# Optimization experiments

Hardware: AMD Instinct MI355X
Metric: run time of the kernel (lower is better)

Reference implementation:

```python
import jax, jax.numpy as jnp
import numpy as np

N_NODES = 100000


def gcn_conv(x, src, dst, norm, W, b, n_nodes):
    # x: [N, Din]; src/dst: [E'] (with self-loops); norm: [E']
    h = x @ W  # [N, Dout] dense transform first (PyG GCNConv order)
    msgs = h[src] * norm[:, None]  # gather + degree scaling, [E', Dout]
    out = jax.ops.segment_sum(msgs, dst, num_segments=n_nodes)  # scatter-add
    return out + b


def setup_inputs() -> dict:
    key = jax.random.key(0)
    k_x, k_e, k_w1, k_w2 = jax.random.split(key, 4)
    input_dim, hidden_dim = 256, 128
    n_edges = 1600000
    x = jax.random.normal(k_x, (N_NODES, input_dim), dtype=jnp.float32)
    edge_index = jax.random.randint(k_e, (2, n_edges), 0, N_NODES, dtype=jnp.int64)
    # Glorot-style init for conv weights, zeros bias (PyG defaults)
    s1 = (6.0 / (input_dim + hidden_dim)) ** 0.5
    s2 = (6.0 / (hidden_dim + hidden_dim)) ** 0.5
    W1 = jax.random.uniform(k_w1, (input_dim, hidden_dim), jnp.float32, -s1, s1)
    W2 = jax.random.uniform(k_w2, (hidden_dim, hidden_dim), jnp.float32, -s2, s2)
    b1 = jnp.zeros((hidden_dim,), jnp.float32)
    b2 = jnp.zeros((hidden_dim,), jnp.float32)
    return {"x": x, "edge_index": edge_index, "W1": W1, "b1": b1, "W2": W2, "b2": b2}


def reference(x, edge_index, W1, b1, W2, b2):
    n = x.shape[0]
    loops = jnp.arange(n, dtype=edge_index.dtype)
    src = jnp.concatenate([edge_index[0], loops])  # add self-loops
    dst = jnp.concatenate([edge_index[1], loops])
    # symmetric normalization deg^-1/2 (in-degree including self-loops)
    deg = jax.ops.segment_sum(jnp.ones_like(dst, dtype=x.dtype), dst, num_segments=n)
    dinv = jax.lax.rsqrt(deg)
    norm = dinv[src] * dinv[dst]
    # layer 1: GCNConv -> ReLU (dropout is identity in eval mode)
    h = jax.nn.relu(gcn_conv(x, src, dst, norm, W1, b1, n))
    # layer 2
    h = jax.nn.relu(gcn_conv(h, src, dst, norm, W2, b2, n))
    return h
```

## Files before the change

### kernel.cpp

```cpp
#include <hip/hip_runtime.h>
#include <hip/hip_bf16.h>


#define DIN 256
#define DH 128
#define BKT_SHIFT 9
#define BKT_SZ 512
#define NBKT_MAX 256
#define CAP 10240

typedef __attribute__((ext_vector_type(8))) short short8;
typedef __attribute__((ext_vector_type(4))) float f32x4;
typedef __attribute__((ext_vector_type(2))) unsigned int uint2e;

__device__ __forceinline__ unsigned short f2bf(float f) {
    union { float f; unsigned int i; } c;
    c.f = f;
    unsigned int r = c.i + 0x7FFFu + ((c.i >> 16) & 1u);
    return (unsigned short)(r >> 16);
}
__device__ __forceinline__ float bf_lo(unsigned int u) {
    union { unsigned int i; float f; } c;
    c.i = u << 16;
    return c.f;
}
__device__ __forceinline__ float bf_hi(unsigned int u) {
    union { unsigned int i; float f; } c;
    c.i = u & 0xFFFF0000u;
    return c.f;
}

__global__ __launch_bounds__(256) void cvt_zero_k(const float* __restrict__ W1,
                                                  const float* __restrict__ W2,
                                                  unsigned short* __restrict__ Wt1,
                                                  unsigned short* __restrict__ Wt2,
                                                  int* __restrict__ bcnt, int WTB) {
    int bx = blockIdx.x;
    int t = threadIdx.x;
    if (bx >= WTB) {
        bcnt[t] = 0;
        return;
    }
    int i = bx * 256 + t;
    if (i < 256 * 128) {
        int k = i >> 7, nn = i & 127;
        Wt1[(size_t)nn * 256 + k] = f2bf(W1[i]);
    } else {
        int j = i - 256 * 128;
        int k = j >> 7, nn = j & 127;
        Wt2[(size_t)nn * 128 + k] = f2bf(W2[j]);
    }
}

template <bool A_BF16, bool SCALE>
__device__ __forceinline__ void gemm_body(unsigned short* Bt, int gb,
                                          const void* __restrict__ Av,
                                          const unsigned short* __restrict__ Wt,
                                          const float* __restrict__ dinv,
                                          unsigned short* __restrict__ Hb,
                                          int M, int K) {
    const int t = threadIdx.x;
    const int w = t >> 6;
    const int lane = t & 63;
    const int l15 = lane & 15;
    const int quad = lane >> 4;
    const int row0 = gb * 128 + w * 32;

    const float* Af = (const float*)Av;
    const unsigned short* Ab = (const unsigned short*)Av;

    f32x4 acc[2][8];
#pragma unroll
    for (int rt = 0; rt < 2; ++rt)
#pragma unroll
        for (int ct = 0; ct < 8; ++ct)
#pragma unroll
            for (int j = 0; j < 4; ++j) acc[rt][ct][j] = 0.0f;

    for (int kc = 0; kc < K; kc += 128) {
        if (kc) __syncthreads();
#pragma unroll
        for (int i = 0; i < 8; ++i) {
            int fg = w * 8 + i;
            int ks = fg >> 3, ct = fg & 7;
            int nn = ct * 16 + l15;
            int gk = ks * 32 + quad * 8;
            *(short8*)&Bt[fg * 512 + lane * 8] =
                *(const short8*)(Wt + (size_t)nn * K + kc + gk);
        }
        __syncthreads();
#pragma unroll
        for (int ks = 0; ks < 4; ++ks) {
            int kk = ks * 32 + quad * 8;
            short8 af[2];
#pragma unroll
            for (int rt = 0; rt < 2; ++rt) {
                int row = row0 + rt * 16 + l15;
                if (row < M) {
                    if (A_BF16) {
                        af[rt] = *(const short8*)(Ab + (size_t)row * K + kc + kk);
                    } else {
                        const float* p = Af + (size_t)row * K + kc + kk;
                        float4 x0 = *(const float4*)p;
                        float4 x1 = *(const float4*)(p + 4);
                        af[rt][0] = (short)f2bf(x0.x);
                        af[rt][1] = (short)f2bf(x0.y);
                        af[rt][2] = (short)f2bf(x0.z);
                        af[rt][3] = (short)f2bf(x0.w);
                        af[rt][4] = (short)f2bf(x1.x);
                        af[rt][5] = (short)f2bf(x1.y);
                        af[rt][6] = (short)f2bf(x1.z);
                        af[rt][7] = (short)f2bf(x1.w);
                    }
                } else {
#pragma unroll
                    for (int j = 0; j < 8; ++j) af[rt][j] = 0;
                }
            }
#pragma unroll
            for (int ct = 0; ct < 8; ++ct) {
                short8 bfr = *(const short8*)&Bt[(ks * 8 + ct) * 512 + lane * 8];
                acc[0][ct] = __builtin_amdgcn_mfma_f32_16x16x32_bf16(af[0], bfr, acc[0][ct], 0, 0, 0);
                acc[1][ct] = __builtin_amdgcn_mfma_f32_16x16x32_bf16(af[1], bfr, acc[1][ct], 0, 0, 0);
            }
        }
    }
#pragma unroll
    for (int rt = 0; rt < 2; ++rt)
#pragma unroll
        for (int r = 0; r < 4; ++r) {
            int row = row0 + rt * 16 + quad * 4 + r;
            if (row < M) {
                float dv = SCALE ? dinv[row] : 1.0f;
                unsigned short* o = Hb + (size_t)row * 128 + l15;
#pragma unroll
                for (int ct = 0; ct < 8; ++ct)
                    o[ct * 16] = f2bf(SCALE ? dv * acc[rt][ct][r] : acc[rt][ct][r]);
            }
        }
}

struct SmemFused {
    union {
        unsigned short Bt[16384];
        struct {
            int hist[NBKT_MAX];
            int rstart[NBKT_MAX];
        } bk;
    };
};

__global__ __launch_bounds__(256) void fused1_k(const int* __restrict__ src,
                                                const int* __restrict__ dst,
                                                int* __restrict__ bcnt,
                                                int* __restrict__ tmp, int e, int n,
                                                int NBB,
                                                const float* __restrict__ x,
                                                const unsigned short* __restrict__ Wt1,
                                                unsigned short* __restrict__ hb, int M) {
    __shared__ SmemFused sm;
    int bx = blockIdx.x;
    int t = threadIdx.x;
    if (bx < NBB) {
        int* hist = sm.bk.hist;
        int* rstart = sm.bk.rstart;
        int chunk = (e + NBB - 1) / NBB;
        int beg = bx * chunk, end = min(e, beg + chunk);

        hist[t] = 0;
        __syncthreads();
        for (int i = beg + t; i < end; i += 256) atomicAdd(&hist[dst[i] >> BKT_SHIFT], 1);
        __syncthreads();
        int nbkt = (n + BKT_SZ - 1) >> BKT_SHIFT;
        int h = hist[t];
        if (t < nbkt && h > 0) rstart[t] = atomicAdd(&bcnt[t], h);
        __syncthreads();
        hist[t] = 0;
        __syncthreads();
        for (int i = beg + t; i < end; i += 256) {
            int d = dst[i];
            int b = d >> BKT_SHIFT;
            int o = atomicAdd(&hist[b], 1);
            tmp[(size_t)b * CAP + rstart[b] + o] = src[i] | ((d & (BKT_SZ - 1)) << 20);
        }
        return;
    }
    gemm_body<false, false>(sm.Bt, bx - NBB, x, Wt1, nullptr, hb, M, DIN);
}

__global__ __launch_bounds__(1024) void scatter2_k(const int* __restrict__ tmp,
                                                   const int* __restrict__ bcnt,
                                                   float* __restrict__ dinv,
                                                   int* __restrict__ rowptr,
                                                   int* __restrict__ einfo, int n,
                                                   int nbkt) {
    __shared__ int hist[BKT_SZ];
    __shared__ int scn[BKT_SZ];
    __shared__ int cur[BKT_SZ];
    int b = blockIdx.x;
    int t = threadIdx.x;
    int lo = b << BKT_SHIFT;
    int nn = min(n - lo, BKT_SZ);
    int cnt = bcnt[b];
    const int* rec = tmp + (size_t)b * CAP;

    if (t < 256) scn[t] = (t < nbkt) ? bcnt[t] : 0;
    __syncthreads();
    for (int off = 1; off < 256; off <<= 1) {
        int v = 0;
        if (t < 256 && t >= off) v = scn[t - off];
        __syncthreads();
        if (t < 256) scn[t] += v;
        __syncthreads();
    }
    int bas = scn[b] - cnt;
    if (b == nbkt - 1 && t == 0) rowptr[n] = scn[nbkt - 1];
    __syncthreads();

    if (t < BKT_SZ) hist[t] = 0;
    __syncthreads();
    for (int i = t; i < cnt; i += 1024) atomicAdd(&hist[(rec[i] >> 20) & (BKT_SZ - 1)], 1);
    __syncthreads();
    if (t < BKT_SZ) scn[t] = hist[t];
    __syncthreads();
    for (int off = 1; off < BKT_SZ; off <<= 1) {
        int v = 0;
        if (t < BKT_SZ && t >= off) v = scn[t - off];
        __syncthreads();
        if (t < BKT_SZ) scn[t] += v;
        __syncthreads();
    }
    if (t < nn) {
        int excl = bas + scn[t] - hist[t];
        dinv[lo + t] = 1.0f / sqrtf((float)(hist[t] + 1));
        rowptr[lo + t] = excl;
        cur[t] = excl;
    }
    __syncthreads();
    for (int i = t; i < cnt; i += 1024) {
        int r = rec[i];
        int dlow = (r >> 20) & (BKT_SZ - 1);
        int pos = atomicAdd(&cur[dlow], 1);
        einfo[pos] = r & 0xFFFFF;
    }
}

template <bool SCALE_SRC, bool OUT_BF16>
__global__ __launch_bounds__(256) void agg_k(const unsigned short* __restrict__ Hb,
                                             const int* __restrict__ rowptr,
                                             const int* __restrict__ einfo,
                                             const float* __restrict__ dinv,
                                             const float* __restrict__ bias,
                                             void* __restrict__ out, int n) {
    int v = blockIdx.x * 4 + (threadIdx.x >> 6);
    int lane = threadIdx.x & 63;
    if (v >= n) return;
    int l = lane & 31, half = lane >> 5;
    const uint2* __restrict__ H = (const uint2*)Hb;
    float dv = dinv[v];
    float a0 = 0.f, a1 = 0.f, a2 = 0.f, a3 = 0.f;
    if (half == 0) {
        uint2 hv = H[(size_t)v * 32 + l];
        if (SCALE_SRC) {
            a0 = dv * bf_lo(hv.x); a1 = dv * bf_hi(hv.x);
            a2 = dv * bf_lo(hv.y); a3 = dv * bf_hi(hv.y);
        } else {
            a0 = bf_lo(hv.x); a1 = bf_hi(hv.x);
            a2 = bf_lo(hv.y); a3 = bf_hi(hv.y);
        }
    }
    int end = rowptr[v + 1];
    int i = rowptr[v] + half;
    for (; i + 6 < end; i += 8) {
        int s0 = __builtin_nontemporal_load(&einfo[i]);
        int s1 = __builtin_nontemporal_load(&einfo[i + 2]);
        int s2 = __builtin_nontemporal_load(&einfo[i + 4]);
        int s3 = __builtin_nontemporal_load(&einfo[i + 6]);
        float d0 = 1.f, d1 = 1.f, d2 = 1.f, d3 = 1.f;
        if (SCALE_SRC) { d0 = dinv[s0]; d1 = dinv[s1]; d2 = dinv[s2]; d3 = dinv[s3]; }
        uint2 v0 = H[(size_t)s0 * 32 + l];
        uint2 v1 = H[(size_t)s1 * 32 + l];
        uint2 v2 = H[(size_t)s2 * 32 + l];
        uint2 v3 = H[(size_t)s3 * 32 + l];
        if (SCALE_SRC) {
            a0 = fmaf(d0, bf_lo(v0.x), a0); a1 = fmaf(d0, bf_hi(v0.x), a1);
            a2 = fmaf(d0, bf_lo(v0.y), a2); a3 = fmaf(d0, bf_hi(v0.y), a3);
            a0 = fmaf(d1, bf_lo(v1.x), a0); a1 = fmaf(d1, bf_hi(v1.x), a1);
            a2 = fmaf(d1, bf_lo(v1.y), a2); a3 = fmaf(d1, bf_hi(v1.y), a3);
            a0 = fmaf(d2, bf_lo(v2.x), a0); a1 = fmaf(d2, bf_hi(v2.x), a1);
            a2 = fmaf(d2, bf_lo(v2.y), a2); a3 = fmaf(d2, bf_hi(v2.y), a3);
            a0 = fmaf(d3, bf_lo(v3.x), a0); a1 = fmaf(d3, bf_hi(v3.x), a1);
            a2 = fmaf(d3, bf_lo(v3.y), a2); a3 = fmaf(d3, bf_hi(v3.y), a3);
        } else {
            a0 += bf_lo(v0.x); a1 += bf_hi(v0.x); a2 += bf_lo(v0.y); a3 += bf_hi(v0.y);
            a0 += bf_lo(v1.x); a1 += bf_hi(v1.x); a2 += bf_lo(v1.y); a3 += bf_hi(v1.y);
            a0 += bf_lo(v2.x); a1 += bf_hi(v2.x); a2 += bf_lo(v2.y); a3 += bf_hi(v2.y);
            a0 += bf_lo(v3.x); a1 += bf_hi(v3.x); a2 += bf_lo(v3.y); a3 += bf_hi(v3.y);
        }
    }
    for (; i < end; i += 2) {
        int s = __builtin_nontemporal_load(&einfo[i]);
        float ds = SCALE_SRC ? dinv[s] : 1.f;
        uint2 vv = H[(size_t)s * 32 + l];
        if (SCALE_SRC) {
            a0 = fmaf(ds, bf_lo(vv.x), a0); a1 = fmaf(ds, bf_hi(vv.x), a1);
            a2 = fmaf(ds, bf_lo(vv.y), a2); a3 = fmaf(ds, bf_hi(vv.y), a3);
        } else {
            a0 += bf_lo(vv.x); a1 += bf_hi(vv.x); a2 += bf_lo(vv.y); a3 += bf_hi(vv.y);
        }
    }
    a0 += __shfl_xor(a0, 32);
    a1 += __shfl_xor(a1, 32);
    a2 += __shfl_xor(a2, 32);
    a3 += __shfl_xor(a3, 32);
    if (half == 0) {
        float4 bb = ((const float4*)bias)[l];
        float o0 = fmaxf(fmaf(dv, a0, bb.x), 0.f);
        float o1 = fmaxf(fmaf(dv, a1, bb.y), 0.f);
        float o2 = fmaxf(fmaf(dv, a2, bb.z), 0.f);
        float o3 = fmaxf(fmaf(dv, a3, bb.w), 0.f);
        if (OUT_BF16) {
            uint2e p;
            p.x = (unsigned int)f2bf(o0) | ((unsigned int)f2bf(o1) << 16);
            p.y = (unsigned int)f2bf(o2) | ((unsigned int)f2bf(o3) << 16);
            __builtin_nontemporal_store(p, (uint2e*)out + (size_t)v * 32 + l);
        } else {
            f32x4 o = {o0, o1, o2, o3};
            __builtin_nontemporal_store(o, (f32x4*)out + (size_t)v * 32 + l);
        }
    }
}

__global__ __launch_bounds__(256) void gemm2_k(const unsigned short* __restrict__ A,
                                               const unsigned short* __restrict__ Wt,
                                               const float* __restrict__ dinv,
                                               unsigned short* __restrict__ Hb,
                                               int M, int K) {
    __shared__ unsigned short Bt[16384];
    gemm_body<true, true>(Bt, blockIdx.x, A, Wt, dinv, Hb, M, K);
}

static inline size_t align_up(size_t x, size_t a) { return (x + a - 1) & ~(a - 1); }

extern "C" void kernel_launch(void* const* d_in, const int* in_sizes, int n_in,
                              void* d_out, int out_size, void* d_ws, size_t ws_size,
                              hipStream_t stream) {
    const float* x  = (const float*)d_in[0];
    const int*   ei = (const int*)d_in[1];
    const float* W1 = (const float*)d_in[2];
    const float* b1 = (const float*)d_in[3];
    const float* W2 = (const float*)d_in[4];
    const float* b2 = (const float*)d_in[5];

    const int N = in_sizes[0] / DIN;
    const int E = in_sizes[1] / 2;
    const int* src = ei;
    const int* dst = ei + E;
    const int NBKT = (N + BKT_SZ - 1) >> BKT_SHIFT;

    char* base_p = (char*)d_ws;
    size_t off = 0;
    int* bcnt = (int*)(base_p + off);       off = align_up(off + 256 * 4, 256);
    int* rowptr = (int*)(base_p + off);     off = align_up(off + (size_t)(N + 1) * 4, 256);
    float* dinv = (float*)(base_p + off);   off = align_up(off + (size_t)N * 4, 256);
    int* tmp = (int*)(base_p + off);        off = align_up(off + (size_t)NBKT * CAP * 4, 256);
    int* einfo = (int*)(base_p + off);      off = align_up(off + (size_t)E * 4, 256);
    unsigned short* Wt1 = (unsigned short*)(base_p + off); off = align_up(off + (size_t)128 * 256 * 2, 256);
    unsigned short* Wt2 = (unsigned short*)(base_p + off); off = align_up(off + (size_t)128 * 128 * 2, 256);
    unsigned short* hb  = (unsigned short*)(base_p + off); off = align_up(off + (size_t)N * 128 * 2, 256);
    unsigned short* a1b = (unsigned short*)(base_p + off); off = align_up(off + (size_t)N * 128 * 2, 256);

    float* out = (float*)d_out;

    const int NBB = 512;
    const int WTB = (256 * 128 + 128 * 128 + 255) / 256;
    const int GB = (N + 127) / 128;

    cvt_zero_k<<<WTB + 1, 256, 0, stream>>>(W1, W2, Wt1, Wt2, bcnt, WTB);
    fused1_k<<<NBB + GB, 256, 0, stream>>>(src, dst, bcnt, tmp, E, N, NBB, x, Wt1, hb, N);
    scatter2_k<<<NBKT, 1024, 0, stream>>>(tmp, bcnt, dinv, rowptr, einfo, N, NBKT);
    agg_k<true, true><<<(N + 3) / 4, 256, 0, stream>>>(hb, rowptr, einfo, dinv, b1, a1b, N);
    gemm2_k<<<GB, 256, 0, stream>>>(a1b, Wt2, dinv, hb, N, DH);
    agg_k<false, false><<<(N + 3) / 4, 256, 0, stream>>>(hb, rowptr, einfo, dinv, b2, out, N);
}
```

Baseline: 410.8 us.

## Fuse layer-1 aggregation with layer-2 weight GEMM via per-block MFMA

Merges the first aggregation kernel and the second dense transform: each 4-node block aggregates rows into LDS as bf16 and then runs a 16x16x32 MFMA against W2 (rows padded to 16 with zeros), writing dinv-scaled bf16 H2. This removes the separate GEMM launch and the round trip of the layer-1 activations through global memory. In exchange, only 4 of 16 MFMA rows are useful and every block rereads W2 from global/L2. The bucket-counter zeroing also moves to a hipMemsetAsync, which adds a separate operation on the stream.

```diff
diff --git a/kernel.cpp b/kernel.cpp
--- a/kernel.cpp
+++ b/kernel.cpp
@@ -245,29 +245,127 @@
     }
 }
 
-template <bool SCALE_SRC, bool OUT_BF16>
-__global__ __launch_bounds__(256) void agg_k(const unsigned short* __restrict__ Hb,
-                                             const int* __restrict__ rowptr,
-                                             const int* __restrict__ einfo,
-                                             const float* __restrict__ dinv,
-                                             const float* __restrict__ bias,
-                                             void* __restrict__ out, int n) {
+__global__ __launch_bounds__(256, 8) void agg1_w2_k(const unsigned short* __restrict__ Hb,
+                                                    const int* __restrict__ rowptr,
+                                                    const int* __restrict__ einfo,
+                                                    const float* __restrict__ dinv,
+                                                    const float* __restrict__ bias,
+                                                    const unsigned short* __restrict__ Wt2,
+                                                    unsigned short* __restrict__ G2,
+                                                    int n) {
+    __shared__ unsigned short a1s[16][128];
+    int t = threadIdx.x;
+    int wv = t >> 6;
+    int lane = t & 63;
+    int v0 = blockIdx.x * 4;
+    int v = v0 + wv;
+    {
+        unsigned int* z = (unsigned int*)a1s;
+        for (int i = 256 + t; i < 1024; i += 256) z[i] = 0;
+    }
+    int l = lane & 31, half = lane >> 5;
+    const uint2* __restrict__ H = (const uint2*)Hb;
+    bool valid = (v < n);
+    float o0 = 0.f, o1 = 0.f, o2 = 0.f, o3 = 0.f;
+    if (valid) {
+        float dv = dinv[v];
+        float a0 = 0.f, a1 = 0.f, a2 = 0.f, a3 = 0.f;
+        if (half == 0) {
+            uint2 hv = H[(size_t)v * 32 + l];
+            a0 = dv * bf_lo(hv.x); a1 = dv * bf_hi(hv.x);
+            a2 = dv * bf_lo(hv.y); a3 = dv * bf_hi(hv.y);
+        }
+        int end = rowptr[v + 1];
+        int i = rowptr[v] + half;
+        for (; i + 6 < end; i += 8) {
+            int s0 = __builtin_nontemporal_load(&einfo[i]);
+            int s1 = __builtin_nontemporal_load(&einfo[i + 2]);
+            int s2 = __builtin_nontemporal_load(&einfo[i + 4]);
+            int s3 = __builtin_nontemporal_load(&einfo[i + 6]);
+            float d0 = dinv[s0], d1 = dinv[s1], d2 = dinv[s2], d3 = dinv[s3];
+            uint2 v0g = H[(size_t)s0 * 32 + l];
+            uint2 v1g = H[(size_t)s1 * 32 + l];
+            uint2 v2g = H[(size_t)s2 * 32 + l];
+            uint2 v3g = H[(size_t)s3 * 32 + l];
+            a0 = fmaf(d0, bf_lo(v0g.x), a0); a1 = fmaf(d0, bf_hi(v0g.x), a1);
+            a2 = fmaf(d0, bf_lo(v0g.y), a2); a3 = fmaf(d0, bf_hi(v0g.y), a3);
+            a0 = fmaf(d1, bf_lo(v1g.x), a0); a1 = fmaf(d1, bf_hi(v1g.x), a1);
+            a2 = fmaf(d1, bf_lo(v1g.y), a2); a3 = fmaf(d1, bf_hi(v1g.y), a3);
+            a0 = fmaf(d2, bf_lo(v2g.x), a0); a1 = fmaf(d2, bf_hi(v2g.x), a1);
+            a2 = fmaf(d2, bf_lo(v2g.y), a2); a3 = fmaf(d2, bf_hi(v2g.y), a3);
+            a0 = fmaf(d3, bf_lo(v3g.x), a0); a1 = fmaf(d3, bf_hi(v3g.x), a1);
+            a2 = fmaf(d3, bf_lo(v3g.y), a2); a3 = fmaf(d3, bf_hi(v3g.y), a3);
+        }
+        for (; i < end; i += 2) {
+            int s = __builtin_nontemporal_load(&einfo[i]);
+            float ds = dinv[s];
+            uint2 vv = H[(size_t)s * 32 + l];
+            a0 = fmaf(ds, bf_lo(vv.x), a0); a1 = fmaf(ds, bf_hi(vv.x), a1);
+            a2 = fmaf(ds, bf_lo(vv.y), a2); a3 = fmaf(ds, bf_hi(vv.y), a3);
+        }
+        a0 += __shfl_xor(a0, 32);
+        a1 += __shfl_xor(a1, 32);
+        a2 += __shfl_xor(a2, 32);
+        a3 += __shfl_xor(a3, 32);
+        if (half == 0) {
+            float4 bb = ((const float4*)bias)[l];
+            o0 = fmaxf(fmaf(dv, a0, bb.x), 0.f);
+            o1 = fmaxf(fmaf(dv, a1, bb.y), 0.f);
+            o2 = fmaxf(fmaf(dv, a2, bb.z), 0.f);
+            o3 = fmaxf(fmaf(dv, a3, bb.w), 0.f);
+        }
+    }
+    if (half == 0) {
+        unsigned int p0 = (unsigned int)f2bf(o0) | ((unsigned int)f2bf(o1) << 16);
+        unsigned int p1 = (unsigned int)f2bf(o2) | ((unsigned int)f2bf(o3) << 16);
+        unsigned int* rowp = (unsigned int*)a1s[wv];
+        rowp[l * 2] = p0;
+        rowp[l * 2 + 1] = p1;
+    }
+    __syncthreads();
+    const int l15 = lane & 15;
+    const int quad = lane >> 4;
+    const int ct0 = wv, ct1 = wv + 4;
+    f32x4 acc0 = {0.f, 0.f, 0.f, 0.f};
+    f32x4 acc1 = {0.f, 0.f, 0.f, 0.f};
+#pragma unroll
+    for (int ks = 0; ks < 4; ++ks) {
+        int kk = ks * 32 + quad * 8;
+        short8 afr = *(const short8*)&a1s[l15][kk];
+        short8 b0 = *(const short8*)(Wt2 + (size_t)(ct0 * 16 + l15) * 128 + kk);
+        short8 b1 = *(const short8*)(Wt2 + (size_t)(ct1 * 16 + l15) * 128 + kk);
+        acc0 = __builtin_amdgcn_mfma_f32_16x16x32_bf16(afr, b0, acc0, 0, 0, 0);
+        acc1 = __builtin_amdgcn_mfma_f32_16x16x32_bf16(afr, b1, acc1, 0, 0, 0);
+    }
+    if (quad == 0) {
+#pragma unroll
+        for (int j = 0; j < 4; ++j) {
+            int vj = v0 + j;
+            if (vj < n) {
+                float dj = dinv[vj];
+                G2[(size_t)vj * 128 + ct0 * 16 + l15] = f2bf(dj * acc0[j]);
+                G2[(size_t)vj * 128 + ct1 * 16 + l15] = f2bf(dj * acc1[j]);
+            }
+        }
+    }
+}
+
+__global__ __launch_bounds__(256) void agg2_k(const unsigned short* __restrict__ Hb,
+                                              const int* __restrict__ rowptr,
+                                              const int* __restrict__ einfo,
+                                              const float* __restrict__ dinv,
+                                              const float* __restrict__ bias,
+                                              float* __restrict__ out, int n) {
     int v = blockIdx.x * 4 + (threadIdx.x >> 6);
     int lane = threadIdx.x & 63;
     if (v >= n) return;
     int l = lane & 31, half = lane >> 5;
     const uint2* __restrict__ H = (const uint2*)Hb;
-    float dv = dinv[v];
     float a0 = 0.f, a1 = 0.f, a2 = 0.f, a3 = 0.f;
     if (half == 0) {
         uint2 hv = H[(size_t)v * 32 + l];
-        if (SCALE_SRC) {
-            a0 = dv * bf_lo(hv.x); a1 = dv * bf_hi(hv.x);
-            a2 = dv * bf_lo(hv.y); a3 = dv * bf_hi(hv.y);
-        } else {
-            a0 = bf_lo(hv.x); a1 = bf_hi(hv.x);
-            a2 = bf_lo(hv.y); a3 = bf_hi(hv.y);
-        }
+        a0 = bf_lo(hv.x); a1 = bf_hi(hv.x);
+        a2 = bf_lo(hv.y); a3 = bf_hi(hv.y);
     }
     int end = rowptr[v + 1];
     int i = rowptr[v] + half;
@@ -276,68 +374,34 @@
         int s1 = __builtin_nontemporal_load(&einfo[i + 2]);
         int s2 = __builtin_nontemporal_load(&einfo[i + 4]);
         int s3 = __builtin_nontemporal_load(&einfo[i + 6]);
-        float d0 = 1.f, d1 = 1.f, d2 = 1.f, d3 = 1.f;
-        if (SCALE_SRC) { d0 = dinv[s0]; d1 = dinv[s1]; d2 = dinv[s2]; d3 = dinv[s3]; }
         uint2 v0 = H[(size_t)s0 * 32 + l];
         uint2 v1 = H[(size_t)s1 * 32 + l];
         uint2 v2 = H[(size_t)s2 * 32 + l];
         uint2 v3 = H[(size_t)s3 * 32 + l];
-        if (SCALE_SRC) {
-            a0 = fmaf(d0, bf_lo(v0.x), a0); a1 = fmaf(d0, bf_hi(v0.x), a1);
-            a2 = fmaf(d0, bf_lo(v0.y), a2); a3 = fmaf(d0, bf_hi(v0.y), a3);
-            a0 = fmaf(d1, bf_lo(v1.x), a0); a1 = fmaf(d1, bf_hi(v1.x), a1);
-            a2 = fmaf(d1, bf_lo(v1.y), a2); a3 = fmaf(d1, bf_hi(v1.y), a3);
-            a0 = fmaf(d2, bf_lo(v2.x), a0); a1 = fmaf(d2, bf_hi(v2.x), a1);
-            a2 = fmaf(d2, bf_lo(v2.y), a2); a3 = fmaf(d2, bf_hi(v2.y), a3);
-            a0 = fmaf(d3, bf_lo(v3.x), a0); a1 = fmaf(d3, bf_hi(v3.x), a1);
-            a2 = fmaf(d3, bf_lo(v3.y), a2); a3 = fmaf(d3, bf_hi(v3.y), a3);
-        } else {
-            a0 += bf_lo(v0.x); a1 += bf_hi(v0.x); a2 += bf_lo(v0.y); a3 += bf_hi(v0.y);
-            a0 += bf_lo(v1.x); a1 += bf_hi(v1.x); a2 += bf_lo(v1.y); a3 += bf_hi(v1.y);
-            a0 += bf_lo(v2.x); a1 += bf_hi(v2.x); a2 += bf_lo(v2.y); a3 += bf_hi(v2.y);
-            a0 += bf_lo(v3.x); a1 += bf_hi(v3.x); a2 += bf_lo(v3.y); a3 += bf_hi(v3.y);
-        }
+        a0 += bf_lo(v0.x); a1 += bf_hi(v0.x); a2 += bf_lo(v0.y); a3 += bf_hi(v0.y);
+        a0 += bf_lo(v1.x); a1 += bf_hi(v1.x); a2 += bf_lo(v1.y); a3 += bf_hi(v1.y);
+        a0 += bf_lo(v2.x); a1 += bf_hi(v2.x); a2 += bf_lo(v2.y); a3 += bf_hi(v2.y);
+        a0 += bf_lo(v3.x); a1 += bf_hi(v3.x); a2 += bf_lo(v3.y); a3 += bf_hi(v3.y);
     }
     for (; i < end; i += 2) {
         int s = __builtin_nontemporal_load(&einfo[i]);
-        float ds = SCALE_SRC ? dinv[s] : 1.f;
         uint2 vv = H[(size_t)s * 32 + l];
-        if (SCALE_SRC) {
-            a0 = fmaf(ds, bf_lo(vv.x), a0); a1 = fmaf(ds, bf_hi(vv.x), a1);
-            a2 = fmaf(ds, bf_lo(vv.y), a2); a3 = fmaf(ds, bf_hi(vv.y), a3);
-        } else {
-            a0 += bf_lo(vv.x); a1 += bf_hi(vv.x); a2 += bf_lo(vv.y); a3 += bf_hi(vv.y);
-        }
+        a0 += bf_lo(vv.x); a1 += bf_hi(vv.x); a2 += bf_lo(vv.y); a3 += bf_hi(vv.y);
     }
     a0 += __shfl_xor(a0, 32);
     a1 += __shfl_xor(a1, 32);
     a2 += __shfl_xor(a2, 32);
     a3 += __shfl_xor(a3, 32);
     if (half == 0) {
+        float dv = dinv[v];
         float4 bb = ((const float4*)bias)[l];
         float o0 = fmaxf(fmaf(dv, a0, bb.x), 0.f);
         float o1 = fmaxf(fmaf(dv, a1, bb.y), 0.f);
         float o2 = fmaxf(fmaf(dv, a2, bb.z), 0.f);
         float o3 = fmaxf(fmaf(dv, a3, bb.w), 0.f);
-        if (OUT_BF16) {
-            uint2e p;
-            p.x = (unsigned int)f2bf(o0) | ((unsigned int)f2bf(o1) << 16);
-            p.y = (unsigned int)f2bf(o2) | ((unsigned int)f2bf(o3) << 16);
-            __builtin_nontemporal_store(p, (uint2e*)out + (size_t)v * 32 + l);
-        } else {
-            f32x4 o = {o0, o1, o2, o3};
-            __builtin_nontemporal_store(o, (f32x4*)out + (size_t)v * 32 + l);
-        }
-    }
-}
-
-__global__ __launch_bounds__(256) void gemm2_k(const unsigned short* __restrict__ A,
-                                               const unsigned short* __restrict__ Wt,
-                                               const float* __restrict__ dinv,
-                                               unsigned short* __restrict__ Hb,
-                                               int M, int K) {
-    __shared__ unsigned short Bt[16384];
-    gemm_body<true, true>(Bt, blockIdx.x, A, Wt, dinv, Hb, M, K);
+        f32x4 o = {o0, o1, o2, o3};
+        __builtin_nontemporal_store(o, (f32x4*)out + (size_t)v * 32 + l);
+    }
 }
 
 static inline size_t align_up(size_t x, size_t a) { return (x + a - 1) & ~(a - 1); }
@@ -368,7 +432,7 @@
     unsigned short* Wt1 = (unsigned short*)(base_p + off); off = align_up(off + (size_t)128 * 256 * 2, 256);
     unsigned short* Wt2 = (unsigned short*)(base_p + off); off = align_up(off + (size_t)128 * 128 * 2, 256);
     unsigned short* hb  = (unsigned short*)(base_p + off); off = align_up(off + (size_t)N * 128 * 2, 256);
-    unsigned short* a1b = (unsigned short*)(base_p + off); off = align_up(off + (size_t)N * 128 * 2, 256);
+    unsigned short* g2b = (unsigned short*)(base_p + off); off = align_up(off + (size_t)N * 128 * 2, 256);
 
     float* out = (float*)d_out;
 
@@ -376,10 +440,10 @@
     const int WTB = (256 * 128 + 128 * 128 + 255) / 256;
     const int GB = (N + 127) / 128;
 
-    cvt_zero_k<<<WTB + 1, 256, 0, stream>>>(W1, W2, Wt1, Wt2, bcnt, WTB);
+    hipMemsetAsync(bcnt, 0, 256 * sizeof(int), stream);
+    cvt_zero_k<<<WTB, 256, 0, stream>>>(W1, W2, Wt1, Wt2, bcnt, WTB);
     fused1_k<<<NBB + GB, 256, 0, stream>>>(src, dst, bcnt, tmp, E, N, NBB, x, Wt1, hb, N);
     scatter2_k<<<NBKT, 1024, 0, stream>>>(tmp, bcnt, dinv, rowptr, einfo, N, NBKT);
-    agg_k<true, true><<<(N + 3) / 4, 256, 0, stream>>>(hb, rowptr, einfo, dinv, b1, a1b, N);
-    gemm2_k<<<GB, 256, 0, stream>>>(a1b, Wt2, dinv, hb, N, DH);
-    agg_k<false, false><<<(N + 3) / 4, 256, 0, stream>>>(hb, rowptr, einfo, dinv, b2, out, N);
-}
+    agg1_w2_k<<<(N + 3) / 4, 256, 0, stream>>>(hb, rowptr, einfo, dinv, b1, Wt2, g2b, N);
+    agg2_k<<<(N + 3) / 4, 256, 0, stream>>>(g2b, rowptr, einfo, dinv, b2, out, N);
+}
```

New measurement: 468.0 us. 13.9% more time.

## Replace bucketed two-pass CSR build with global degree count, scan, atomic scatter

Applied to the files above, without the earlier changes.

The CSR construction no longer stages edges in per-bucket temporary buffers. It now counts per-node in-degree with global atomics (fused alongside the first GEMM), runs a per-bucket scan to build rowptr, cursors and dinv, then scatters each source index into place with one global atomic per edge. This drops the intermediate tmp buffer and its second read, but adds many contended global atomics and an extra memset and kernel launch. Edge order within a row also becomes nondeterministic.

```diff
diff --git a/kernel.cpp b/kernel.cpp
--- a/kernel.cpp
+++ b/kernel.cpp
@@ -7,7 +7,6 @@
 #define BKT_SHIFT 9
 #define BKT_SZ 512
 #define NBKT_MAX 256
-#define CAP 10240
 
 typedef __attribute__((ext_vector_type(8))) short short8;
 typedef __attribute__((ext_vector_type(4))) float f32x4;
@@ -30,22 +29,15 @@
     return c.f;
 }
 
-__global__ __launch_bounds__(256) void cvt_zero_k(const float* __restrict__ W1,
-                                                  const float* __restrict__ W2,
-                                                  unsigned short* __restrict__ Wt1,
-                                                  unsigned short* __restrict__ Wt2,
-                                                  int* __restrict__ bcnt, int WTB) {
-    int bx = blockIdx.x;
-    int t = threadIdx.x;
-    if (bx >= WTB) {
-        bcnt[t] = 0;
-        return;
-    }
-    int i = bx * 256 + t;
+__global__ __launch_bounds__(256) void cvt_k(const float* __restrict__ W1,
+                                             const float* __restrict__ W2,
+                                             unsigned short* __restrict__ Wt1,
+                                             unsigned short* __restrict__ Wt2) {
+    int i = blockIdx.x * 256 + threadIdx.x;
     if (i < 256 * 128) {
         int k = i >> 7, nn = i & 127;
         Wt1[(size_t)nn * 256 + k] = f2bf(W1[i]);
-    } else {
+    } else if (i < 256 * 128 + 128 * 128) {
         int j = i - 256 * 128;
         int k = j >> 7, nn = j & 127;
         Wt2[(size_t)nn * 128 + k] = f2bf(W2[j]);
@@ -143,105 +135,91 @@
 struct SmemFused {
     union {
         unsigned short Bt[16384];
-        struct {
-            int hist[NBKT_MAX];
-            int rstart[NBKT_MAX];
-        } bk;
+        int hist[NBKT_MAX];
     };
 };
 
-__global__ __launch_bounds__(256) void fused1_k(const int* __restrict__ src,
-                                                const int* __restrict__ dst,
-                                                int* __restrict__ bcnt,
-                                                int* __restrict__ tmp, int e, int n,
-                                                int NBB,
-                                                const float* __restrict__ x,
-                                                const unsigned short* __restrict__ Wt1,
-                                                unsigned short* __restrict__ hb, int M) {
+__global__ __launch_bounds__(256) void fused_a(const int* __restrict__ dst,
+                                               int* __restrict__ deg,
+                                               int* __restrict__ bsum,
+                                               int e, int n, int DEGB,
+                                               const float* __restrict__ x,
+                                               const unsigned short* __restrict__ Wt1,
+                                               unsigned short* __restrict__ hb, int M) {
     __shared__ SmemFused sm;
     int bx = blockIdx.x;
     int t = threadIdx.x;
-    if (bx < NBB) {
-        int* hist = sm.bk.hist;
-        int* rstart = sm.bk.rstart;
-        int chunk = (e + NBB - 1) / NBB;
+    if (bx < DEGB) {
+        int nbkt = (n + BKT_SZ - 1) >> BKT_SHIFT;
+        int chunk = (e + DEGB - 1) / DEGB;
         int beg = bx * chunk, end = min(e, beg + chunk);
-
-        hist[t] = 0;
-        __syncthreads();
-        for (int i = beg + t; i < end; i += 256) atomicAdd(&hist[dst[i] >> BKT_SHIFT], 1);
-        __syncthreads();
-        int nbkt = (n + BKT_SZ - 1) >> BKT_SHIFT;
-        int h = hist[t];
-        if (t < nbkt && h > 0) rstart[t] = atomicAdd(&bcnt[t], h);
-        __syncthreads();
-        hist[t] = 0;
+        sm.hist[t] = 0;
         __syncthreads();
         for (int i = beg + t; i < end; i += 256) {
             int d = dst[i];
-            int b = d >> BKT_SHIFT;
-            int o = atomicAdd(&hist[b], 1);
-            tmp[(size_t)b * CAP + rstart[b] + o] = src[i] | ((d & (BKT_SZ - 1)) << 20);
-        }
+            atomicAdd(&deg[d], 1);
+            atomicAdd(&sm.hist[d >> BKT_SHIFT], 1);
+        }
+        __syncthreads();
+        int h = sm.hist[t];
+        if (t < nbkt && h > 0) atomicAdd(&bsum[t], h);
         return;
     }
-    gemm_body<false, false>(sm.Bt, bx - NBB, x, Wt1, nullptr, hb, M, DIN);
-}
-
-__global__ __launch_bounds__(1024) void scatter2_k(const int* __restrict__ tmp,
-                                                   const int* __restrict__ bcnt,
-                                                   float* __restrict__ dinv,
-                                                   int* __restrict__ rowptr,
-                                                   int* __restrict__ einfo, int n,
-                                                   int nbkt) {
-    __shared__ int hist[BKT_SZ];
-    __shared__ int scn[BKT_SZ];
-    __shared__ int cur[BKT_SZ];
+    gemm_body<false, false>(sm.Bt, bx - DEGB, x, Wt1, nullptr, hb, M, DIN);
+}
+
+__global__ __launch_bounds__(512) void scan_k(const int* __restrict__ deg,
+                                              const int* __restrict__ bsum,
+                                              int* __restrict__ rowptr,
+                                              int* __restrict__ cur,
+                                              float* __restrict__ dinv,
+                                              int n, int nbkt) {
+    __shared__ int s196[256];
+    __shared__ int sc[512];
     int b = blockIdx.x;
     int t = threadIdx.x;
     int lo = b << BKT_SHIFT;
     int nn = min(n - lo, BKT_SZ);
-    int cnt = bcnt[b];
-    const int* rec = tmp + (size_t)b * CAP;
-
-    if (t < 256) scn[t] = (t < nbkt) ? bcnt[t] : 0;
+
+    if (t < 256) s196[t] = (t < nbkt) ? bsum[t] : 0;
     __syncthreads();
     for (int off = 1; off < 256; off <<= 1) {
         int v = 0;
-        if (t < 256 && t >= off) v = scn[t - off];
-        __syncthreads();
-        if (t < 256) scn[t] += v;
-        __syncthreads();
-    }
-    int bas = scn[b] - cnt;
-    if (b == nbkt - 1 && t == 0) rowptr[n] = scn[nbkt - 1];
+        if (t < 256 && t >= off) v = s196[t - off];
+        __syncthreads();
+        if (t < 256) s196[t] += v;
+        __syncthreads();
+    }
+    int bas = (b == 0) ? 0 : s196[b - 1];
+    if (b == nbkt - 1 && t == 0) rowptr[n] = s196[nbkt - 1];
+
+    int dv_ = (t < nn) ? deg[lo + t] : 0;
+    sc[t] = dv_;
     __syncthreads();
-
-    if (t < BKT_SZ) hist[t] = 0;
-    __syncthreads();
-    for (int i = t; i < cnt; i += 1024) atomicAdd(&hist[(rec[i] >> 20) & (BKT_SZ - 1)], 1);
-    __syncthreads();
-    if (t < BKT_SZ) scn[t] = hist[t];
-    __syncthreads();
-    for (int off = 1; off < BKT_SZ; off <<= 1) {
+    for (int off = 1; off < 512; off <<= 1) {
         int v = 0;
-        if (t < BKT_SZ && t >= off) v = scn[t - off];
-        __syncthreads();
-        if (t < BKT_SZ) scn[t] += v;
+        if (t >= off) v = sc[t - off];
+        __syncthreads();
+        sc[t] += v;
         __syncthreads();
     }
     if (t < nn) {
-        int excl = bas + scn[t] - hist[t];
-        dinv[lo + t] = 1.0f / sqrtf((float)(hist[t] + 1));
+        int excl = bas + sc[t] - dv_;
         rowptr[lo + t] = excl;
-        cur[t] = excl;
-    }
-    __syncthreads();
-    for (int i = t; i < cnt; i += 1024) {
-        int r = rec[i];
-        int dlow = (r >> 20) & (BKT_SZ - 1);
-        int pos = atomicAdd(&cur[dlow], 1);
-        einfo[pos] = r & 0xFFFFF;
+        cur[lo + t] = excl;
+        dinv[lo + t] = 1.0f / sqrtf((float)(dv_ + 1));
+    }
+}
+
+__global__ __launch_bounds__(256) void scatter_k(const int* __restrict__ src,
+                                                 const int* __restrict__ dst,
+                                                 int* __restrict__ cur,
+                                                 int* __restrict__ einfo, int e) {
+    int i = blockIdx.x * 256 + threadIdx.x;
+    if (i < e) {
+        int d = dst[i];
+        int pos = atomicAdd(&cur[d], 1);
+        einfo[pos] = src[i];
     }
 }
 
@@ -360,10 +338,11 @@
 
     char* base_p = (char*)d_ws;
     size_t off = 0;
-    int* bcnt = (int*)(base_p + off);       off = align_up(off + 256 * 4, 256);
+    int* deg = (int*)(base_p + off);        off = align_up(off + (size_t)(N + 256) * 4, 256);
+    int* bsum = deg + N;
     int* rowptr = (int*)(base_p + off);     off = align_up(off + (size_t)(N + 1) * 4, 256);
+    int* cur = (int*)(base_p + off);        off = align_up(off + (size_t)N * 4, 256);
     float* dinv = (float*)(base_p + off);   off = align_up(off + (size_t)N * 4, 256);
-    int* tmp = (int*)(base_p + off);        off = align_up(off + (size_t)NBKT * CAP * 4, 256);
     int* einfo = (int*)(base_p + off);      off = align_up(off + (size_t)E * 4, 256);
     unsigned short* Wt1 = (unsigned short*)(base_p + off); off = align_up(off + (size_t)128 * 256 * 2, 256);
     unsigned short* Wt2 = (unsigned short*)(base_p + off); off = align_up(off + (size_t)128 * 128 * 2, 256);
@@ -372,13 +351,15 @@
 
     float* out = (float*)d_out;
 
-    const int NBB = 512;
+    const int DEGB = 512;
     const int WTB = (256 * 128 + 128 * 128 + 255) / 256;
     const int GB = (N + 127) / 128;
 
-    cvt_zero_k<<<WTB + 1, 256, 0, stream>>>(W1, W2, Wt1, Wt2, bcnt, WTB);
-    fused1_k<<<NBB + GB, 256, 0, stream>>>(src, dst, bcnt, tmp, E, N, NBB, x, Wt1, hb, N);
-    scatter2_k<<<NBKT, 1024, 0, stream>>>(tmp, bcnt, dinv, rowptr, einfo, N, NBKT);
+    hipMemsetAsync(deg, 0, (size_t)(N + 256) * sizeof(int), stream);
+    cvt_k<<<WTB, 256, 0, stream>>>(W1, W2, Wt1, Wt2);
+    fused_a<<<DEGB + GB, 256, 0, stream>>>(dst, deg, bsum, E, N, DEGB, x, Wt1, hb, N);
+    scan_k<<<NBKT, 512, 0, stream>>>(deg, bsum, rowptr, cur, dinv, N, NBKT);
+    scatter_k<<<(E + 255) / 256, 256, 0, stream>>>(src, dst, cur, einfo, E);
     agg_k<true, true><<<(N + 3) / 4, 256, 0, stream>>>(hb, rowptr, einfo, dinv, b1, a1b, N);
     gemm2_k<<<GB, 256, 0, stream>>>(a1b, Wt2, dinv, hb, N, DH);
     agg_k<false, false><<<(N + 3) / 4, 256, 0, stream>>>(hb, rowptr, einfo, dinv, b2, out, N);
```

After: 557.5 us. 1.36x slower.
